# Optimization experiments

Hardware: AMD Instinct MI355X
Metric: run time of the kernel (lower is better)

The kernel has to match this reference:

```python
import jax, jax.numpy as jnp
import numpy as np

B, E, D, NH, NP = 4, 32, 1024, 16, 4
LQ = E * E
DH = D // NH


def layer_norm(x, g, b, eps=1e-6):
    m = x.mean(-1, keepdims=True)
    v = ((x - m) ** 2).mean(-1, keepdims=True)
    return (x - m) / jnp.sqrt(v + eps) * g + b


def get_ref(H, W):
    # matches MSCrossAttnBlock.get_reference_points: centers normalized to [0,1], (x, y) order
    ys, xs = jnp.meshgrid((jnp.arange(H, dtype=jnp.float32) + 0.5) / H,
                          (jnp.arange(W, dtype=jnp.float32) + 0.5) / W, indexing='ij')
    return jnp.stack([xs.ravel(), ys.ravel()], -1)  # (H*W, 2)


def bilinear_sample(value_l, loc, H, W):
    # value_l: (N, nH, H*W, dh); loc: (N, Lq, nH, P, 2) normalized to [0,1]
    # replicates F.grid_sample(align_corners=False, padding_mode='zeros') with grid = 2*loc - 1
    N, Lq, nH, P, _ = loc.shape
    x = loc[..., 0] * W - 0.5
    y = loc[..., 1] * H - 0.5
    x0 = jnp.floor(x)
    y0 = jnp.floor(y)
    wx1 = x - x0
    wy1 = y - y0
    out = 0.0
    for dy, wy in ((0, 1.0 - wy1), (1, wy1)):
        for dx, wx in ((0, 1.0 - wx1), (1, wx1)):
            xi = x0 + dx
            yi = y0 + dy
            valid = (xi >= 0) & (xi < W) & (yi >= 0) & (yi < H)
            idx = (jnp.clip(yi, 0, H - 1) * W + jnp.clip(xi, 0, W - 1)).astype(jnp.int32)
            idx_t = idx.transpose(0, 2, 1, 3).reshape(N, nH, Lq * P)  # (N, nH, Lq*P)
            g = jnp.take_along_axis(value_l, idx_t[..., None], axis=2)  # (N, nH, Lq*P, dh)
            g = g.reshape(N, nH, Lq, P, -1).transpose(0, 2, 1, 3, 4)  # (N, Lq, nH, P, dh)
            w = (wx * wy) * valid.astype(value_l.dtype)
            out = out + g * w[..., None]
    return out


def msdeform(query, ref, inp, shapes, Wv, bv, Wo, bo, Wa, ba, Wp, bp):
    # MSDeformAttn forward (no padding mask)
    N, Lq, d = query.shape
    nL = len(shapes)
    value = (inp @ Wv.T + bv).reshape(N, -1, NH, DH).transpose(0, 2, 1, 3)  # (N, nH, Lin, dh)
    off = (query @ Wo.T + bo).reshape(N, Lq, NH, nL, NP, 2)
    attw = jax.nn.softmax((query @ Wa.T + ba).reshape(N, Lq, NH, nL * NP), axis=-1)
    attw = attw.reshape(N, Lq, NH, nL, NP)
    normalizer = jnp.array([[w, h] for (h, w) in shapes], dtype=query.dtype)  # (nL, 2) = [W, H]
    loc = ref[None, :, None, None, None, :] + off / normalizer[None, None, None, :, None, :]
    out = 0.0
    start = 0
    for l, (H, W) in enumerate(shapes):
        sampled = bilinear_sample(value[:, :, start:start + H * W], loc[:, :, :, l], H, W)
        out = out + (sampled * attw[:, :, :, l, :, None]).sum(3)  # (N, Lq, nH, dh)
        start += H * W
    return out.reshape(N, Lq, d) @ Wp.T + bp


def setup_inputs() -> dict:
    key = jax.random.key(0)
    ks = iter(jax.random.split(key, 64))
    def rnd(shape, scale):
        return jax.random.normal(next(ks), shape, dtype=jnp.float32) * scale
    inp = {}
    for i in range(4):
        inp[f'src{i}'] = rnd((B, LQ, D), 1.0)
    for nm in ('qn', 'fn', 'n1'):
        inp[nm + '_g'] = jnp.ones((D,), jnp.float32)
        inp[nm + '_b'] = jnp.zeros((D,), jnp.float32)
    inp['gamma1'] = rnd((D,), 0.1)
    inp['gamma2'] = rnd((D,), 0.1)
    ws = D ** -0.5
    for pre, nl in (('ca', 4), ('sa', 1)):
        inp[pre + '_vw'] = rnd((D, D), ws)
        inp[pre + '_vb'] = jnp.zeros((D,), jnp.float32)
        inp[pre + '_ow'] = rnd((NH * nl * NP * 2, D), ws)
        inp[pre + '_ob'] = rnd((NH * nl * NP * 2,), 0.1)
        inp[pre + '_aw'] = rnd((NH * nl * NP, D), ws)
        inp[pre + '_ab'] = jnp.zeros((NH * nl * NP,), jnp.float32)
        inp[pre + '_pw'] = rnd((D, D), ws)
        inp[pre + '_pb'] = jnp.zeros((D,), jnp.float32)
    return inp


def reference(src0, src1, src2, src3, qn_g, qn_b, fn_g, fn_b, n1_g, n1_b, gamma1, gamma2,
              ca_vw, ca_vb, ca_ow, ca_ob, ca_aw, ca_ab, ca_pw, ca_pb,
              sa_vw, sa_vb, sa_ow, sa_ob, sa_aw, sa_ab, sa_pw, sa_pb):
    shapes4 = [(E, E)] * 4
    feat = jnp.concatenate([src0, src1, src2, src3], axis=1)  # (B, 4*LQ, D)
    query = src3  # srcs[-1], pos embed is None
    ref = get_ref(E, E)  # (LQ, 2)
    attn = msdeform(layer_norm(query, qn_g, qn_b), ref, layer_norm(feat, fn_g, fn_b),
                    shapes4, ca_vw, ca_vb, ca_ow, ca_ob, ca_aw, ca_ab, ca_pw, ca_pb)
    attn1 = layer_norm(attn, n1_g, n1_b)
    attn2 = msdeform(attn1, ref, attn1, [(E, E)],
                     sa_vw, sa_vb, sa_ow, sa_ob, sa_aw, sa_ab, sa_pw, sa_pb)
    attn = attn + gamma2 * attn2
    return query + gamma1 * attn
```

## Files before the change

### kernel.cpp

```cpp
#include <hip/hip_runtime.h>


#define DEV __device__ __forceinline__

typedef float f32x4 __attribute__((ext_vector_type(4)));
typedef __bf16 bf16x8 __attribute__((ext_vector_type(8)));

DEV unsigned short f2bf(float f) {
  union { float f; unsigned u; } a; a.f = f;
  unsigned r = a.u + 0x7fffu + ((a.u >> 16) & 1u);
  return (unsigned short)(r >> 16);
}
DEV float bf2f(unsigned short h) {
  union { unsigned u; float f; } a; a.u = ((unsigned)h) << 16;
  return a.f;
}

struct CvtArgs {
  const float* src[8];
  unsigned short* dst;
  int off4[9];
};

__global__ __launch_bounds__(256) void f2bf_multi(CvtArgs a) {
  int i = blockIdx.x * 256 + threadIdx.x;
  int seg = 0;
  #pragma unroll
  for (int s = 1; s < 8; ++s) seg += (i >= a.off4[s]) ? 1 : 0;
  const float4 v = ((const float4*)a.src[seg])[i - a.off4[seg]];
  unsigned short* o = a.dst + (size_t)i * 4;
  o[0] = f2bf(v.x); o[1] = f2bf(v.y); o[2] = f2bf(v.z); o[3] = f2bf(v.w);
}

DEV void ln_row_wave(const float* __restrict__ xr, const float* __restrict__ g,
                     const float* __restrict__ b,
                     unsigned short* __restrict__ op_row) {
  const int lane = threadIdx.x & 63;
  float4 v[4];
  float s = 0.f, s2 = 0.f;
  #pragma unroll
  for (int j = 0; j < 4; ++j) {
    v[j] = ((const float4*)xr)[lane + 64 * j];
    s  += v[j].x + v[j].y + v[j].z + v[j].w;
    s2 += v[j].x*v[j].x + v[j].y*v[j].y + v[j].z*v[j].z + v[j].w*v[j].w;
  }
  #pragma unroll
  for (int o = 32; o; o >>= 1) { s += __shfl_xor(s, o); s2 += __shfl_xor(s2, o); }
  const float mean = s * (1.f / 1024.f);
  const float rstd = rsqrtf(s2 * (1.f / 1024.f) - mean * mean + 1e-6f);
  #pragma unroll
  for (int j = 0; j < 4; ++j) {
    float4 gg = ((const float4*)g)[lane + 64 * j];
    float4 bb = ((const float4*)b)[lane + 64 * j];
    ushort4 r;
    r.x = f2bf((v[j].x - mean) * rstd * gg.x + bb.x);
    r.y = f2bf((v[j].y - mean) * rstd * gg.y + bb.y);
    r.z = f2bf((v[j].z - mean) * rstd * gg.z + bb.z);
    r.w = f2bf((v[j].w - mean) * rstd * gg.w + bb.w);
    ((ushort4*)op_row)[lane + 64 * j] = r;
  }
}

__global__ __launch_bounds__(256) void ln_wave_kernel(
    const float* __restrict__ x, const float* __restrict__ g,
    const float* __restrict__ b, unsigned short* __restrict__ out) {
  int row = blockIdx.x * 4 + (threadIdx.x >> 6);
  ln_row_wave(x + (size_t)row * 1024, g, b, out + (size_t)row * 1024);
}

__global__ __launch_bounds__(256) void ln5_wave_kernel(
    const float* __restrict__ s0, const float* __restrict__ s1,
    const float* __restrict__ s2, const float* __restrict__ s3,
    const float* __restrict__ fg, const float* __restrict__ fb,
    const float* __restrict__ qg, const float* __restrict__ qb,
    unsigned short* __restrict__ f_out, unsigned short* __restrict__ q_out) {
  int row = blockIdx.x * 4 + (threadIdx.x >> 6);
  if (row < 16384) {
    int l = row >> 12, inner = row & 4095;
    const float* srcs[4] = {s0, s1, s2, s3};
    int orow = (inner >> 10) * 4096 + l * 1024 + (inner & 1023);
    ln_row_wave(srcs[l] + (size_t)inner * 1024, fg, fb,
                f_out + (size_t)orow * 1024);
  } else {
    int inner = row - 16384;
    ln_row_wave(s3 + (size_t)inner * 1024, qg, qb,
                q_out + (size_t)inner * 1024);
  }
}

struct GemmP {
  const unsigned short* A; const unsigned short* W;
  void* C; void* C1; void* C2;
  const float* b0; const float* b1; const float* b2;
  const float* src3; const float* g1; const float* g2; const float* attnp;
  int M, N, K, tilesM;
};

template <int BM, int BN, int EPI>
DEV void gemm_body(const GemmP& P, int id, unsigned short* sA,
                   unsigned short* sB) {
  constexpr int WMT = BM / 2, WNT = BN / 2;
  constexpr int MF = WMT / 16, NF = WNT / 16;
  constexpr int PA = BM / 64, PB = BN / 64;
  const int tid = threadIdx.x;
  const int wave = tid >> 6, lane = tid & 63;
  const int wm = (wave & 1) * WMT, wn = (wave >> 1) * WNT;
  const int m0 = (id % P.tilesM) * BM;
  const int n0 = (id / P.tilesM) * BN;
  const int lq = lane >> 4, lm = lane & 15;
  const int r16 = lane >> 2;
  const int cst = lane & 3;
  const int csrc = cst ^ ((r16 >> 1) & 3);
  const int aslot = lq ^ ((lm >> 1) & 3);

  f32x4 acc[MF][NF] = {};
  bf16x8 ald[2][PA], bld[2][PB];

  #pragma unroll 1
  for (int k0 = 0; k0 < P.K; k0 += 64) {
    #pragma unroll
    for (int s = 0; s < 2; ++s) {
      #pragma unroll
      for (int p = 0; p < PA; ++p) {
        int grow = m0 + (wave + 4 * p) * 16 + r16;
        ald[s][p] = *(const bf16x8*)(P.A + (size_t)grow * P.K + k0 + s * 32 + csrc * 8);
      }
      #pragma unroll
      for (int p = 0; p < PB; ++p) {
        int grow = min(n0 + (wave + 4 * p) * 16 + r16, P.N - 1);
        bld[s][p] = *(const bf16x8*)(P.W + (size_t)grow * P.K + k0 + s * 32 + csrc * 8);
      }
    }
    __syncthreads();
    #pragma unroll
    for (int s = 0; s < 2; ++s) {
      #pragma unroll
      for (int p = 0; p < PA; ++p)
        *(bf16x8*)(sA + s * BM * 32 + (wave + 4 * p) * 512 + (r16 * 4 + cst) * 8) = ald[s][p];
      #pragma unroll
      for (int p = 0; p < PB; ++p)
        *(bf16x8*)(sB + s * BN * 32 + (wave + 4 * p) * 512 + (r16 * 4 + cst) * 8) = bld[s][p];
    }
    __syncthreads();
    #pragma unroll
    for (int s = 0; s < 2; ++s) {
      bf16x8 af[MF], bfr[NF];
      #pragma unroll
      for (int mi = 0; mi < MF; ++mi)
        af[mi] = *(const bf16x8*)(sA + s * BM * 32 + ((wm >> 4) + mi) * 512 + lm * 32 + aslot * 8);
      #pragma unroll
      for (int ni = 0; ni < NF; ++ni)
        bfr[ni] = *(const bf16x8*)(sB + s * BN * 32 + ((wn >> 4) + ni) * 512 + lm * 32 + aslot * 8);
      #pragma unroll
      for (int mi = 0; mi < MF; ++mi)
        #pragma unroll
        for (int ni = 0; ni < NF; ++ni)
          acc[mi][ni] = __builtin_amdgcn_mfma_f32_16x16x32_bf16(
              af[mi], bfr[ni], acc[mi][ni], 0, 0, 0);
    }
  }

  #pragma unroll
  for (int mi = 0; mi < MF; ++mi) {
    #pragma unroll
    for (int ni = 0; ni < NF; ++ni) {
      const int col = n0 + wn + ni * 16 + lm;
      #pragma unroll
      for (int r2 = 0; r2 < 4; ++r2) {
        const int row = m0 + wm + mi * 16 + lq * 4 + r2;
        float v = acc[mi][ni][r2];
        if constexpr (EPI == 0) {
          ((float*)P.C)[(size_t)row * 1024 + col] = v + P.b0[col];
        } else if constexpr (EPI == 1) {
          ((unsigned short*)P.C)[(size_t)row * 1024 + col] = f2bf(v + P.b0[col]);
        } else if constexpr (EPI == 2) {
          if (col < 512)
            ((float*)P.C)[(size_t)row * 512 + col] = v + P.b0[col];
          else
            ((float*)P.C1)[(size_t)row * 256 + col - 512] = v + P.b1[col - 512];
        } else if constexpr (EPI == 3) {
          if (col < 1024)
            ((unsigned short*)P.C)[(size_t)row * 1024 + col] = f2bf(v + P.b0[col]);
          else if (col < 1152)
            ((float*)P.C1)[(size_t)row * 128 + col - 1024] = v + P.b1[col - 1024];
          else if (col < 1216)
            ((float*)P.C2)[(size_t)row * 64 + col - 1152] = v + P.b2[col - 1152];
        } else {
          size_t i = (size_t)row * 1024 + col;
          float vv = v + P.b0[col];
          ((float*)P.C)[i] = P.src3[i] + P.g1[col] * (P.attnp[i] + P.g2[col] * vv);
        }
      }
    }
  }
}

template <int BM, int BN, int EPI>
__global__ __launch_bounds__(256) void gemm_v3(GemmP P) {
  extern __shared__ __align__(16) unsigned short smem[];
  gemm_body<BM, BN, EPI>(P, blockIdx.x, smem, smem + BM * 64);
}

template <int BM, int BN>
__global__ __launch_bounds__(256) void gemm_dual(GemmP Pv, GemmP Po, int split) {
  extern __shared__ __align__(16) unsigned short smem[];
  if ((int)blockIdx.x < split)
    gemm_body<BM, BN, 1>(Pv, blockIdx.x, smem, smem + BM * 64);
  else
    gemm_body<BM, BN, 2>(Po, blockIdx.x - split, smem, smem + BM * 64);
}

template <int NLEV>
__global__ __launch_bounds__(256) void ms_sample_fused(
    const unsigned short* __restrict__ value, const float* __restrict__ off,
    const float* __restrict__ logits, unsigned short* __restrict__ out) {
  const int nq = blockIdx.x;
  const int wave = threadIdx.x >> 6, lane = threadIdx.x & 63;
  const int h = (wave << 2) + (lane >> 4);
  const int c = (lane & 15) << 2;
  const int q = nq & 1023, n = nq >> 10;
  const float* offp = off + ((size_t)nq * 16 + h) * (NLEV * 8);
  const float* lgp  = logits + ((size_t)nq * 16 + h) * (NLEV * 4);

  float lg[NLEV * 4];
  #pragma unroll
  for (int i = 0; i < NLEV; ++i) {
    float4 v = ((const float4*)lgp)[i];
    lg[4*i] = v.x; lg[4*i+1] = v.y; lg[4*i+2] = v.z; lg[4*i+3] = v.w;
  }
  float mx = lg[0];
  #pragma unroll
  for (int i = 1; i < NLEV * 4; ++i) mx = fmaxf(mx, lg[i]);
  float ssum = 0.f;
  #pragma unroll
  for (int i = 0; i < NLEV * 4; ++i) { lg[i] = __expf(lg[i] - mx); ssum += lg[i]; }
  const float inv = 1.f / ssum;

  const float fqx = (float)(q & 31), fqy = (float)(q >> 5);
  float a0 = 0.f, a1 = 0.f, a2 = 0.f, a3 = 0.f;

  #pragma unroll
  for (int l = 0; l < NLEV; ++l) {
    const unsigned short* vl =
        value + ((size_t)(n * NLEV + l) << 20) + h * 64 + c;
    #pragma unroll
    for (int p = 0; p < 4; ++p) {
      float2 o2 = ((const float2*)offp)[l * 4 + p];
      float aw = lg[l * 4 + p] * inv;
      float xx = fqx + o2.x, yy = fqy + o2.y;
      float xf = floorf(xx), yf = floorf(yy);
      float fx = xx - xf, fy = yy - yf;
      int ix = (int)xf, iy = (int)yf;
      int ix1 = ix + 1, iy1 = iy + 1;
      float vx0 = ((unsigned)ix  < 32u) ? 1.f : 0.f;
      float vx1 = ((unsigned)ix1 < 32u) ? 1.f : 0.f;
      float vy0 = ((unsigned)iy  < 32u) ? 1.f : 0.f;
      float vy1 = ((unsigned)iy1 < 32u) ? 1.f : 0.f;
      int cx0 = min(max(ix, 0), 31), cx1 = min(max(ix1, 0), 31);
      int cy0 = min(max(iy, 0), 31), cy1 = min(max(iy1, 0), 31);
      float w00 = (1.f - fx) * (1.f - fy) * vx0 * vy0 * aw;
      float w01 = fx * (1.f - fy) * vx1 * vy0 * aw;
      float w10 = (1.f - fx) * fy * vx0 * vy1 * aw;
      float w11 = fx * fy * vx1 * vy1 * aw;
      ushort4 u00 = *(const ushort4*)(vl + ((size_t)(cy0 * 32 + cx0) << 10));
      ushort4 u01 = *(const ushort4*)(vl + ((size_t)(cy0 * 32 + cx1) << 10));
      ushort4 u10 = *(const ushort4*)(vl + ((size_t)(cy1 * 32 + cx0) << 10));
      ushort4 u11 = *(const ushort4*)(vl + ((size_t)(cy1 * 32 + cx1) << 10));
      a0 += w00 * bf2f(u00.x) + w01 * bf2f(u01.x) + w10 * bf2f(u10.x) + w11 * bf2f(u11.x);
      a1 += w00 * bf2f(u00.y) + w01 * bf2f(u01.y) + w10 * bf2f(u10.y) + w11 * bf2f(u11.y);
      a2 += w00 * bf2f(u00.z) + w01 * bf2f(u01.z) + w10 * bf2f(u10.z) + w11 * bf2f(u11.z);
      a3 += w00 * bf2f(u00.w) + w01 * bf2f(u01.w) + w10 * bf2f(u10.w) + w11 * bf2f(u11.w);
    }
  }
  ushort4 r;
  r.x = f2bf(a0); r.y = f2bf(a1); r.z = f2bf(a2); r.w = f2bf(a3);
  *(ushort4*)(out + ((size_t)nq * 16 + h) * 64 + c) = r;
}

extern "C" void kernel_launch(void* const* d_in, const int* in_sizes, int n_in,
                              void* d_out, int out_size, void* d_ws,
                              size_t ws_size, hipStream_t stream) {
  (void)in_sizes; (void)n_in; (void)out_size; (void)ws_size;
  const float* src[4] = {(const float*)d_in[0], (const float*)d_in[1],
                         (const float*)d_in[2], (const float*)d_in[3]};
  const float* qn_g = (const float*)d_in[4];
  const float* qn_b = (const float*)d_in[5];
  const float* fn_g = (const float*)d_in[6];
  const float* fn_b = (const float*)d_in[7];
  const float* n1_g = (const float*)d_in[8];
  const float* n1_b = (const float*)d_in[9];
  const float* gamma1 = (const float*)d_in[10];
  const float* gamma2 = (const float*)d_in[11];
  const float* ca_vw = (const float*)d_in[12];
  const float* ca_vb = (const float*)d_in[13];
  const float* ca_ow = (const float*)d_in[14];
  const float* ca_ob = (const float*)d_in[15];
  const float* ca_aw = (const float*)d_in[16];
  const float* ca_ab = (const float*)d_in[17];
  const float* ca_pw = (const float*)d_in[18];
  const float* ca_pb = (const float*)d_in[19];
  const float* sa_vw = (const float*)d_in[20];
  const float* sa_vb = (const float*)d_in[21];
  const float* sa_ow = (const float*)d_in[22];
  const float* sa_ob = (const float*)d_in[23];
  const float* sa_aw = (const float*)d_in[24];
  const float* sa_ab = (const float*)d_in[25];
  const float* sa_pw = (const float*)d_in[26];
  const float* sa_pb = (const float*)d_in[27];

  char* wsp = (char*)d_ws;
  size_t off = 0;
  auto alloc = [&](size_t bytes) {
    char* r = wsp + off;
    off = (off + bytes + 255) & ~(size_t)255;
    return r;
  };
  const size_t MB = 1024 * 1024;
  unsigned short* w_ca_vw = (unsigned short*)alloc(1024 * 1024 * 2);
  unsigned short* w_ca_ow = (unsigned short*)alloc(512 * 1024 * 2);
  unsigned short* w_ca_aw = (unsigned short*)alloc(256 * 1024 * 2);
  unsigned short* w_ca_pw = (unsigned short*)alloc(1024 * 1024 * 2);
  unsigned short* w_sa_vw = (unsigned short*)alloc(1024 * 1024 * 2);
  unsigned short* w_sa_ow = (unsigned short*)alloc(128 * 1024 * 2);
  unsigned short* w_sa_aw = (unsigned short*)alloc(64 * 1024 * 2);
  unsigned short* w_sa_pw = (unsigned short*)alloc(1024 * 1024 * 2);
  (void)w_ca_aw; (void)w_sa_ow; (void)w_sa_aw;
  char* R1 = alloc(32 * MB);
  char* R2 = alloc(32 * MB);
  char* R3 = alloc(8 * MB);
  char* R4 = alloc(8 * MB);
  char* R5 = alloc(4 * MB);

  unsigned short* f_ln    = (unsigned short*)R1;
  float*          attn    = (float*)R1;
  unsigned short* attn1   = (unsigned short*)(R1 + 16 * MB);
  unsigned short* samp_sa = (unsigned short*)(R1 + 24 * MB);
  unsigned short* val_ca  = (unsigned short*)R2;
  unsigned short* val_sa  = (unsigned short*)R2;
  unsigned short* q_ln    = (unsigned short*)R3;
  unsigned short* samp_ca = (unsigned short*)R3;
  float*          off_ca  = (float*)R4;
  float*          off_sa  = (float*)R4;
  float*          attw_sa = (float*)(R4 + 4 * MB);
  float*          attw_ca = (float*)R5;

  CvtArgs ca;
  ca.src[0] = ca_vw; ca.src[1] = ca_ow; ca.src[2] = ca_aw; ca.src[3] = ca_pw;
  ca.src[4] = sa_vw; ca.src[5] = sa_ow; ca.src[6] = sa_aw; ca.src[7] = sa_pw;
  ca.dst = w_ca_vw;
  const int sizes4[8] = {262144, 131072, 65536, 262144, 262144, 32768, 16384, 262144};
  ca.off4[0] = 0;
  for (int i = 0; i < 8; ++i) ca.off4[i + 1] = ca.off4[i] + sizes4[i];
  f2bf_multi<<<ca.off4[8] / 256, 256, 0, stream>>>(ca);

  ln5_wave_kernel<<<5120, 256, 0, stream>>>(src[0], src[1], src[2], src[3],
                                            fn_g, fn_b, qn_g, qn_b, f_ln, q_ln);

  auto mkP = [](const unsigned short* A, const unsigned short* W, void* C,
                const float* b0, int M, int N, int K, int tilesM) {
    GemmP p{}; p.A = A; p.W = W; p.C = C; p.b0 = b0;
    p.M = M; p.N = N; p.K = K; p.tilesM = tilesM;
    return p;
  };

  {
    GemmP pv = mkP(f_ln, w_ca_vw, val_ca, ca_vb, 16384, 1024, 1024, 128);
    GemmP po = mkP(q_ln, w_ca_ow, off_ca, ca_ob, 4096, 768, 1024, 32);
    po.C1 = attw_ca; po.b1 = ca_ab;
    gemm_dual<128, 128><<<1024 + 192, 256, 65536 / 2, stream>>>(pv, po, 1024);
  }

  ms_sample_fused<4><<<4096, 256, 0, stream>>>(val_ca, off_ca, attw_ca, samp_ca);
  gemm_v3<64, 128, 0><<<64 * 8, 256, (64 + 128) * 64 * 2, stream>>>(
      mkP(samp_ca, w_ca_pw, attn, ca_pb, 4096, 1024, 1024, 64));

  ln_wave_kernel<<<1024, 256, 0, stream>>>(attn, n1_g, n1_b, attn1);
  {
    GemmP p = mkP(attn1, w_sa_vw, val_sa, sa_vb, 4096, 1216, 1024, 64);
    p.C1 = off_sa; p.b1 = sa_ob; p.C2 = attw_sa; p.b2 = sa_ab;
    gemm_v3<64, 128, 3><<<64 * 10, 256, (64 + 128) * 64 * 2, stream>>>(p);
  }
  ms_sample_fused<1><<<4096, 256, 0, stream>>>(val_sa, off_sa, attw_sa, samp_sa);
  {
    GemmP p = mkP(samp_sa, w_sa_pw, d_out, sa_pb, 4096, 1024, 1024, 64);
    p.src3 = src[3]; p.g1 = gamma1; p.g2 = gamma2; p.attnp = attn;
    gemm_v3<64, 128, 4><<<64 * 8, 256, (64 + 128) * 64 * 2, stream>>>(p);
  }
}
```

Before: 356.0 us.

## Double-buffer GEMM K-loop with direct global-to-LDS async loads

```diff
diff --git a/kernel.cpp b/kernel.cpp
--- a/kernel.cpp
+++ b/kernel.cpp
@@ -14,6 +14,12 @@
 DEV float bf2f(unsigned short h) {
   union { unsigned u; float f; } a; a.u = ((unsigned)h) << 16;
   return a.f;
+}
+
+DEV void gl_lds16(const unsigned short* g, unsigned short* l) {
+  __builtin_amdgcn_global_load_lds(
+      (const __attribute__((address_space(1))) void*)g,
+      (__attribute__((address_space(3))) void*)l, 16, 0, 0);
 }
 
 struct CvtArgs {
@@ -97,11 +103,11 @@
 };
 
 template <int BM, int BN, int EPI>
-DEV void gemm_body(const GemmP& P, int id, unsigned short* sA,
-                   unsigned short* sB) {
+DEV void gemm_body(const GemmP& P, int id, unsigned short* smem) {
   constexpr int WMT = BM / 2, WNT = BN / 2;
   constexpr int MF = WMT / 16, NF = WNT / 16;
   constexpr int PA = BM / 64, PB = BN / 64;
+  constexpr int BUF = (BM + BN) * 64;
   const int tid = threadIdx.x;
   const int wave = tid >> 6, lane = tid & 63;
   const int wm = (wave & 1) * WMT, wn = (wave >> 1) * WNT;
@@ -114,43 +120,55 @@
   const int aslot = lq ^ ((lm >> 1) & 3);
 
   f32x4 acc[MF][NF] = {};
-  bf16x8 ald[2][PA], bld[2][PB];
-
-  #pragma unroll 1
-  for (int k0 = 0; k0 < P.K; k0 += 64) {
+  const int kTiles = P.K >> 6;
+
+  const unsigned short* gA[PA];
+  #pragma unroll
+  for (int p = 0; p < PA; ++p) {
+    int grow = m0 + (wave + 4 * p) * 16 + r16;
+    gA[p] = P.A + (size_t)grow * P.K + csrc * 8;
+  }
+  const unsigned short* gB[PB];
+  #pragma unroll
+  for (int p = 0; p < PB; ++p) {
+    int grow = min(n0 + (wave + 4 * p) * 16 + r16, P.N - 1);
+    gB[p] = P.W + (size_t)grow * P.K + csrc * 8;
+  }
+
+  auto stage = [&](int b, int t) {
+    unsigned short* bA = smem + b * BUF;
+    unsigned short* bB = bA + BM * 64;
+    const int k0 = t << 6;
     #pragma unroll
     for (int s = 0; s < 2; ++s) {
       #pragma unroll
-      for (int p = 0; p < PA; ++p) {
-        int grow = m0 + (wave + 4 * p) * 16 + r16;
-        ald[s][p] = *(const bf16x8*)(P.A + (size_t)grow * P.K + k0 + s * 32 + csrc * 8);
-      }
-      #pragma unroll
-      for (int p = 0; p < PB; ++p) {
-        int grow = min(n0 + (wave + 4 * p) * 16 + r16, P.N - 1);
-        bld[s][p] = *(const bf16x8*)(P.W + (size_t)grow * P.K + k0 + s * 32 + csrc * 8);
-      }
+      for (int p = 0; p < PA; ++p)
+        gl_lds16(gA[p] + k0 + s * 32,
+                 bA + s * BM * 32 + (wave + 4 * p) * 512);
+      #pragma unroll
+      for (int p = 0; p < PB; ++p)
+        gl_lds16(gB[p] + k0 + s * 32,
+                 bB + s * BN * 32 + (wave + 4 * p) * 512);
     }
-    __syncthreads();
-    #pragma unroll
-    for (int s = 0; s < 2; ++s) {
-      #pragma unroll
-      for (int p = 0; p < PA; ++p)
-        *(bf16x8*)(sA + s * BM * 32 + (wave + 4 * p) * 512 + (r16 * 4 + cst) * 8) = ald[s][p];
-      #pragma unroll
-      for (int p = 0; p < PB; ++p)
-        *(bf16x8*)(sB + s * BN * 32 + (wave + 4 * p) * 512 + (r16 * 4 + cst) * 8) = bld[s][p];
-    }
-    __syncthreads();
+  };
+
+  stage(0, 0);
+  __syncthreads();
+  int cur = 0;
+  #pragma unroll 1
+  for (int t = 0; t < kTiles; ++t) {
+    if (t + 1 < kTiles) stage(cur ^ 1, t + 1);
+    const unsigned short* bA = smem + cur * BUF;
+    const unsigned short* bB = bA + BM * 64;
     #pragma unroll
     for (int s = 0; s < 2; ++s) {
       bf16x8 af[MF], bfr[NF];
       #pragma unroll
       for (int mi = 0; mi < MF; ++mi)
-        af[mi] = *(const bf16x8*)(sA + s * BM * 32 + ((wm >> 4) + mi) * 512 + lm * 32 + aslot * 8);
+        af[mi] = *(const bf16x8*)(bA + s * BM * 32 + ((wm >> 4) + mi) * 512 + lm * 32 + aslot * 8);
       #pragma unroll
       for (int ni = 0; ni < NF; ++ni)
-        bfr[ni] = *(const bf16x8*)(sB + s * BN * 32 + ((wn >> 4) + ni) * 512 + lm * 32 + aslot * 8);
+        bfr[ni] = *(const bf16x8*)(bB + s * BN * 32 + ((wn >> 4) + ni) * 512 + lm * 32 + aslot * 8);
       #pragma unroll
       for (int mi = 0; mi < MF; ++mi)
         #pragma unroll
@@ -158,6 +176,8 @@
           acc[mi][ni] = __builtin_amdgcn_mfma_f32_16x16x32_bf16(
               af[mi], bfr[ni], acc[mi][ni], 0, 0, 0);
     }
+    __syncthreads();
+    cur ^= 1;
   }
 
   #pragma unroll
@@ -198,16 +218,16 @@
 template <int BM, int BN, int EPI>
 __global__ __launch_bounds__(256) void gemm_v3(GemmP P) {
   extern __shared__ __align__(16) unsigned short smem[];
-  gemm_body<BM, BN, EPI>(P, blockIdx.x, smem, smem + BM * 64);
+  gemm_body<BM, BN, EPI>(P, blockIdx.x, smem);
 }
 
 template <int BM, int BN>
 __global__ __launch_bounds__(256) void gemm_dual(GemmP Pv, GemmP Po, int split) {
   extern __shared__ __align__(16) unsigned short smem[];
   if ((int)blockIdx.x < split)
-    gemm_body<BM, BN, 1>(Pv, blockIdx.x, smem, smem + BM * 64);
+    gemm_body<BM, BN, 1>(Pv, blockIdx.x, smem);
   else
-    gemm_body<BM, BN, 2>(Po, blockIdx.x - split, smem, smem + BM * 64);
+    gemm_body<BM, BN, 2>(Po, blockIdx.x - split, smem);
 }
 
 template <int NLEV>
@@ -363,27 +383,30 @@
     return p;
   };
 
+  constexpr int LDS_128 = 2 * (128 + 128) * 64 * 2;
+  constexpr int LDS_64  = 2 * (64 + 128) * 64 * 2;
+
   {
     GemmP pv = mkP(f_ln, w_ca_vw, val_ca, ca_vb, 16384, 1024, 1024, 128);
     GemmP po = mkP(q_ln, w_ca_ow, off_ca, ca_ob, 4096, 768, 1024, 32);
     po.C1 = attw_ca; po.b1 = ca_ab;
-    gemm_dual<128, 128><<<1024 + 192, 256, 65536 / 2, stream>>>(pv, po, 1024);
+    gemm_dual<128, 128><<<1024 + 192, 256, LDS_128, stream>>>(pv, po, 1024);
   }
 
   ms_sample_fused<4><<<4096, 256, 0, stream>>>(val_ca, off_ca, attw_ca, samp_ca);
-  gemm_v3<64, 128, 0><<<64 * 8, 256, (64 + 128) * 64 * 2, stream>>>(
+  gemm_v3<64, 128, 0><<<64 * 8, 256, LDS_64, stream>>>(
       mkP(samp_ca, w_ca_pw, attn, ca_pb, 4096, 1024, 1024, 64));
 
   ln_wave_kernel<<<1024, 256, 0, stream>>>(attn, n1_g, n1_b, attn1);
   {
     GemmP p = mkP(attn1, w_sa_vw, val_sa, sa_vb, 4096, 1216, 1024, 64);
     p.C1 = off_sa; p.b1 = sa_ob; p.C2 = attw_sa; p.b2 = sa_ab;
-    gemm_v3<64, 128, 3><<<64 * 10, 256, (64 + 128) * 64 * 2, stream>>>(p);
+    gemm_v3<64, 128, 3><<<64 * 10, 256, LDS_64, stream>>>(p);
   }
   ms_sample_fused<1><<<4096, 256, 0, stream>>>(val_sa, off_sa, attw_sa, samp_sa);
   {
     GemmP p = mkP(samp_sa, w_sa_pw, d_out, sa_pb, 4096, 1024, 1024, 64);
     p.src3 = src[3]; p.g1 = gamma1; p.g2 = gamma2; p.attnp = attn;
-    gemm_v3<64, 128, 4><<<64 * 8, 256, (64 + 128) * 64 * 2, stream>>>(p);
-  }
-}
+    gemm_v3<64, 128, 4><<<64 * 8, 256, LDS_64, stream>>>(p);
+  }
+}
```

Result: no change. 356.5 us (+0.1%).
